# Kernel optimization log

Measured on AMD Instinct MI355X. Metric: run time of the kernel, lower is better.

The kernel has to match this reference:

```python
import jax, jax.numpy as jnp
import numpy as np

B, S, N = 64, 256, 512


def setup_inputs() -> dict:
    key = jax.random.key(0)
    ks = jax.random.split(key, 8)
    x = jax.random.normal(ks[0], (B, S, N), dtype=jnp.float32)
    # sparse adjacency, no self loops (module assumes adj has no self-loop)
    adj = (jax.random.uniform(ks[1], (N, N)) < 0.05).astype(jnp.float32)
    adj = adj * (1.0 - jnp.eye(N, dtype=jnp.float32))
    W = jax.random.uniform(ks[2], (N, N), dtype=jnp.float32)  # torch.rand init
    parent_node_weigh = jax.random.uniform(ks[3], (N,), dtype=jnp.float32)
    bound = 1.0 / np.sqrt(N)  # torch Linear default init
    Wq_w = jax.random.uniform(ks[4], (N, N), minval=-bound, maxval=bound, dtype=jnp.float32)
    Wq_b = jax.random.uniform(ks[5], (N,), minval=-bound, maxval=bound, dtype=jnp.float32)
    Wk_w = jax.random.uniform(ks[6], (N, N), minval=-bound, maxval=bound, dtype=jnp.float32)
    Wk_b = jax.random.uniform(ks[7], (N,), minval=-bound, maxval=bound, dtype=jnp.float32)
    return {"x": x, "adj": adj, "W": W, "parent_node_weigh": parent_node_weigh,
            "Wq_w": Wq_w, "Wq_b": Wq_b, "Wk_w": Wk_w, "Wk_b": Wk_b}


def reference(x, adj, W, parent_node_weigh, Wq_w, Wq_b, Wk_w, Wk_b):
    # x: (B,S,N). Q,K = Linear(x).permute(0,2,1) -> (B,N,S)
    Q = jnp.einsum('bsk,nk->bns', x, Wq_w) + Wq_b[None, :, None]
    K = jnp.einsum('bsk,nk->bns', x, Wk_w) + Wk_b[None, :, None]
    xt = jnp.transpose(x, (0, 2, 1))  # (B,N,S)
    n = adj.shape[0]
    # Algebraic equivalent of the repeat/mask/matmul/bmm chain:
    # Att[b,m,n] = adj[m,n] * sum_j W[m,j] * adj[j,n] * <K[b,j,:], Q[b,n,:]>
    S_kq = jnp.einsum('bjs,bns->bjn', K, Q)  # (B,N,N)
    Att = adj * jnp.einsum('mj,bjn->bmn', W, adj[:, :, None].transpose(2, 0, 1)[0][None] * S_kq if False else adj[None, :, :] * S_kq)
    Att = Att + jnp.diag(parent_node_weigh)[None, :, :]
    cycle_adj = jnp.eye(n, dtype=adj.dtype) + adj
    Att = jax.nn.softmax(Att, axis=1) * cycle_adj  # softmax over dim=1 (torch dim=1)
    agg_x = jnp.einsum('bmn,bms->bns', Att, xt)  # Att^T @ x
    return (agg_x, Att)
```

## Files before the change

### kernel.cpp

```cpp
#include <hip/hip_runtime.h>
#include <hip/hip_fp16.h>
#include <cstdint>
#include <cmath>

#define BB 64
#define SS 256
#define NN 512
#define MAXC 64

typedef float f32x4 __attribute__((ext_vector_type(4)));
typedef _Float16 half8 __attribute__((ext_vector_type(8)));

__device__ __forceinline__ unsigned short f2h(float f) {
  return __half_as_ushort(__float2half(f));
}
__device__ __forceinline__ float h2f(unsigned short u) {
  return __half2float(__ushort_as_half(u));
}
__device__ __forceinline__ float2 unpackh2(uint32_t u) {
  return make_float2(__half2float(__ushort_as_half((unsigned short)(u & 0xffffu))),
                     __half2float(__ushort_as_half((unsigned short)(u >> 16))));
}

__device__ __forceinline__ void gload_lds16(const void* g, void* s) {
  __builtin_amdgcn_global_load_lds(
      (const __attribute__((address_space(1))) uint32_t*)g,
      (__attribute__((address_space(3))) uint32_t*)s, 16, 0, 0);
}

__global__ __launch_bounds__(256) void k_collist(const float* __restrict__ adj,
                                                 int* __restrict__ col_idx,
                                                 int* __restrict__ col_cnt) {
  const int n = blockIdx.x * 4 + (threadIdx.x >> 6);
  const int lane = threadIdx.x & 63;
  int cnt = 0;
  for (int m0 = 0; m0 < NN; m0 += 64) {
    const int m = m0 + lane;
    const float a = adj[(size_t)m * NN + n];
    unsigned long long mask = __ballot(a != 0.0f);
    const int prefix = __popcll(mask & ((1ull << lane) - 1ull));
    if (a != 0.0f && cnt + prefix < MAXC) col_idx[n * MAXC + cnt + prefix] = m;
    cnt += __popcll(mask);
  }
  if (lane == 0) col_cnt[n] = (cnt > MAXC) ? MAXC : cnt;
}

__global__ __launch_bounds__(256) void k_wsub(const float* __restrict__ W,
                                              const int* __restrict__ col_idx,
                                              const int* __restrict__ col_cnt,
                                              int* __restrict__ col_off,
                                              float* __restrict__ Wsub) {
  const int n = blockIdx.x;
  const int t = threadIdx.x;
  const int wave = t >> 6, lane = t & 63;
  __shared__ int lsh[MAXC];
  __shared__ int preSh;
  const int c = col_cnt[n];
  if (wave == 0) {
    int pre = 0;
#pragma unroll
    for (int i0 = 0; i0 < NN; i0 += 64) {
      const int i = i0 + lane;
      const int cc = col_cnt[i];
      pre += (i < n) ? cc * cc : 0;
    }
#pragma unroll
    for (int off = 32; off; off >>= 1) pre += __shfl_xor(pre, off);
    if (lane == 0) { col_off[n] = pre; preSh = pre; }
    if (lane < c) lsh[lane] = col_idx[n * MAXC + lane];
  }
  __syncthreads();
  if (lane < c) {
    const float* Wm = W + (size_t)lsh[lane] * NN;
    float* dst = Wsub + preSh + lane;
    for (int ji = wave; ji < c; ji += 4)
      dst[(size_t)ji * c] = Wm[lsh[ji]];
  }
}

__global__ __launch_bounds__(256) void k_xprep(const float* __restrict__ x,
                                               unsigned short* __restrict__ xp,
                                               unsigned short* __restrict__ xt,
                                               float* __restrict__ Att) {
  __shared__ float tile[32][33];
  const int b = blockIdx.z;
  const int s0 = blockIdx.x * 32, n0 = blockIdx.y * 32;
  const float* xb = x + (size_t)b * SS * NN;
  const int tx = threadIdx.x, ty = threadIdx.y;
#pragma unroll
  for (int i = ty; i < 32; i += 8) {
    const float v = xb[(size_t)(s0 + i) * NN + n0 + tx];
    tile[i][tx] = v;
    xp[(size_t)(b * SS + s0 + i) * 512 + n0 + tx] = f2h(v);
  }
  {
    const int bid = (blockIdx.z * 16 + blockIdx.y) * 8 + blockIdx.x;
    const int t = ty * 32 + tx;
    f32x4* dst = (f32x4*)(Att + (size_t)bid * 2048);
    const f32x4 z = (f32x4)0.0f;
    dst[t] = z;
    dst[t + 256] = z;
  }
  __syncthreads();
  unsigned short* xtb = xt + (size_t)b * NN * SS;
#pragma unroll
  for (int i = ty; i < 32; i += 8)
    xtb[(size_t)(n0 + i) * SS + s0 + tx] = f2h(tile[tx][i]);
}

__global__ __launch_bounds__(128) void k_wsplit(const float* __restrict__ Wq,
                                                const float* __restrict__ Wk,
                                                unsigned short* __restrict__ Wqp,
                                                unsigned short* __restrict__ Wkp) {
  const int n = blockIdx.x;
  const float* src = blockIdx.y ? Wk : Wq;
  unsigned short* dst = blockIdx.y ? Wkp : Wqp;
  const int k = threadIdx.x * 4;
  float4 v = *(const float4*)(src + (size_t)n * NN + k);
  ushort4 o;
  o.x = f2h(v.x); o.y = f2h(v.y); o.z = f2h(v.z); o.w = f2h(v.w);
  *(ushort4*)(dst + (size_t)n * 512 + k) = o;
}

__global__ __launch_bounds__(256, 2) void k_lin2(const unsigned short* __restrict__ Wqp,
                                                 const unsigned short* __restrict__ Wkp,
                                                 const float* __restrict__ bq,
                                                 const float* __restrict__ bk,
                                                 const unsigned short* __restrict__ xp,
                                                 unsigned short* __restrict__ Qt,
                                                 unsigned short* __restrict__ Kt) {
  __shared__ __align__(16) char sm[49152];
  const int t = threadIdx.x;
  const int w = t >> 6, l = t & 63;
  const int id = blockIdx.x;
  const int xcd = id & 7, sub = id >> 3;
  const int bn0 = (xcd * 16 + (sub >> 2)) * 128;
  const int bm0 = (sub & 3) * 128;

  const int swz = (((l & 3) ^ ((l >> 3) & 3))) * 16;
  const char* srcb[6];
  char* dstb[6];
#pragma unroll
  for (int i = 0; i < 6; i++) {
    const int ch = w * 6 + i;
    const int panel = ch >> 3, rowgrp = ch & 7;
    const int row = rowgrp * 16 + (l >> 2);
    const char* g0 = (panel == 0) ? (const char*)Wqp
                   : (panel == 1) ? (const char*)Wkp : (const char*)xp;
    const int gr = ((panel == 2) ? bn0 : bm0) + row;
    srcb[i] = g0 + (size_t)gr * 1024 + swz;
    dstb[i] = sm + panel * 8192 + rowgrp * 1024 + l * 16;
  }

  const int fr = l & 15, fg = l >> 4;
  const int mrow = (w >> 1) * 64, ncol = (w & 1) * 64;
  const int slot = (fg ^ ((fr >> 1) & 3)) * 16;
  int offQ[4], offK[4], offB[4];
#pragma unroll
  for (int fm = 0; fm < 4; fm++) {
    offQ[fm] = (mrow + fm * 16 + fr) * 64 + slot;
    offK[fm] = 8192 + (mrow + fm * 16 + fr) * 64 + slot;
    offB[fm] = 16384 + (ncol + fm * 16 + fr) * 64 + slot;
  }

  f32x4 accq[4][4], acck[4][4];
#pragma unroll
  for (int i = 0; i < 4; i++)
#pragma unroll
    for (int j = 0; j < 4; j++) { accq[i][j] = (f32x4)0.0f; acck[i][j] = (f32x4)0.0f; }

#pragma unroll
  for (int i = 0; i < 6; i++) gload_lds16(srcb[i], dstb[i]);
  __syncthreads();

  int cur = 0;
  for (int kk = 0; kk < 16; kk++) {
    if (kk + 1 < 16) {
      const int ko = (kk + 1) * 64;
      const int boff = (cur ^ 1) * 24576;
#pragma unroll
      for (int i = 0; i < 6; i++)
        gload_lds16(srcb[i] + ko, dstb[i] + boff);
    }
    const char* base = sm + cur * 24576;
    half8 afq[4], afk[4];
#pragma unroll
    for (int fm = 0; fm < 4; fm++) {
      afq[fm] = *(const half8*)(base + offQ[fm]);
      afk[fm] = *(const half8*)(base + offK[fm]);
    }
#pragma unroll
    for (int fn = 0; fn < 4; fn++) {
      const half8 bv = *(const half8*)(base + offB[fn]);
#pragma unroll
      for (int fm = 0; fm < 4; fm++) {
        accq[fm][fn] = __builtin_amdgcn_mfma_f32_16x16x32_f16(afq[fm], bv, accq[fm][fn], 0, 0, 0);
        acck[fm][fn] = __builtin_amdgcn_mfma_f32_16x16x32_f16(afk[fm], bv, acck[fm][fn], 0, 0, 0);
      }
    }
    __syncthreads();
    cur ^= 1;
  }

  const int b = bn0 >> 8;
  const int sbase = (bn0 & 255) + ncol;
#pragma unroll
  for (int fm = 0; fm < 4; fm++) {
#pragma unroll
    for (int q = 0; q < 4; q++) {
      const int n = bm0 + mrow + fm * 16 + fg * 4 + q;
      const float bvq = bq[n];
      const float bvk = bk[n];
#pragma unroll
      for (int fn = 0; fn < 4; fn++) {
        const int s = sbase + fn * 16 + fr;
        Qt[((size_t)b * NN + n) * SS + s] = f2h(accq[fm][fn][q] + bvq);
        Kt[((size_t)b * NN + n) * SS + s] = f2h(acck[fm][fn][q] + bvk);
      }
    }
  }
}

__global__ __launch_bounds__(256, 2) void k_gram(const unsigned short* __restrict__ Qt,
                                                 const unsigned short* __restrict__ Kt,
                                                 unsigned short* __restrict__ ST) {
  __shared__ __align__(16) char sm[32768];
  const int t = threadIdx.x;
  const int w = t >> 6, l = t & 63;
  const int id = blockIdx.x;
  const int xcd = id & 7, rest = id >> 3;
  const int batch = (xcd << 3) + (rest >> 4);
  const int tile = rest & 15;
  const int m0 = (tile >> 2) * 128;
  const int n0 = (tile & 3) * 128;

  const int swz = (((l & 3) ^ ((l >> 3) & 3))) * 16;
  const char* srcb[4];
  char* dstb[4];
#pragma unroll
  for (int i = 0; i < 4; i++) {
    const int ch = w * 4 + i;
    const int panel = ch >> 3, rowgrp = ch & 7;
    const int row = rowgrp * 16 + (l >> 2);
    const char* g0 = panel ? (const char*)Kt : (const char*)Qt;
    const int gr = (panel ? n0 : m0) + row;
    srcb[i] = g0 + ((size_t)batch * 512 + gr) * 512 + swz;
    dstb[i] = sm + panel * 8192 + rowgrp * 1024 + l * 16;
  }

  const int fr = l & 15, fg = l >> 4;
  const int mrow = (w >> 1) * 64, ncol = (w & 1) * 64;
  const int slot = (fg ^ ((fr >> 1) & 3)) * 16;
  int offA[4], offB[4];
#pragma unroll
  for (int fm = 0; fm < 4; fm++) {
    offA[fm] = (mrow + fm * 16 + fr) * 64 + slot;
    offB[fm] = 8192 + (ncol + fm * 16 + fr) * 64 + slot;
  }

  f32x4 acc[4][4];
#pragma unroll
  for (int i = 0; i < 4; i++)
#pragma unroll
    for (int j = 0; j < 4; j++) acc[i][j] = (f32x4)0.0f;

#pragma unroll
  for (int i = 0; i < 4; i++) gload_lds16(srcb[i], dstb[i]);
  __syncthreads();

  int cur = 0;
  for (int kk = 0; kk < 8; kk++) {
    if (kk + 1 < 8) {
      const int ko = (kk + 1) * 64;
      const int boff = (cur ^ 1) * 16384;
#pragma unroll
      for (int i = 0; i < 4; i++)
        gload_lds16(srcb[i] + ko, dstb[i] + boff);
    }
    const char* base = sm + cur * 16384;
    half8 af[4];
#pragma unroll
    for (int fm = 0; fm < 4; fm++)
      af[fm] = *(const half8*)(base + offA[fm]);
#pragma unroll
    for (int fn = 0; fn < 4; fn++) {
      const half8 bv = *(const half8*)(base + offB[fn]);
#pragma unroll
      for (int fm = 0; fm < 4; fm++)
        acc[fm][fn] = __builtin_amdgcn_mfma_f32_16x16x32_f16(af[fm], bv, acc[fm][fn], 0, 0, 0);
    }
    __syncthreads();
    cur ^= 1;
  }

  unsigned short* STb = ST + (size_t)batch * NN * NN;
#pragma unroll
  for (int fm = 0; fm < 4; fm++) {
#pragma unroll
    for (int q = 0; q < 4; q++) {
      const int n = m0 + mrow + fm * 16 + fg * 4 + q;
#pragma unroll
      for (int fn = 0; fn < 4; fn++) {
        const int j = n0 + ncol + fn * 16 + fr;
        STb[(size_t)n * NN + j] = f2h(acc[fm][fn][q]);
      }
    }
  }
}

__global__ __launch_bounds__(256) void k_fused(const unsigned short* __restrict__ ST,
                                               const unsigned short* __restrict__ xt,
                                               const float* __restrict__ Wsub,
                                               const float* __restrict__ pnw,
                                               const int* __restrict__ col_idx,
                                               const int* __restrict__ col_cnt,
                                               const int* __restrict__ col_off,
                                               float* __restrict__ Att,
                                               float* __restrict__ agg) {
  const int id = blockIdx.x;
  const int xcd = id & 7;
  const int r = id >> 3;
  const int n = r & 511;
  const int bgrp = r >> 9;
  const int t = threadIdx.x;
  const int wave = t >> 6, lane = t & 63;
  const int b = (xcd << 3) + (bgrp << 2) + wave;

  __shared__ int   lsh[MAXC + 1];
  __shared__ int   lshB[MAXC + 1];
  __shared__ float Wsh[MAXC * MAXC];
  __shared__ float vsh[4][MAXC];
  __shared__ float ash[4][MAXC + 1];

  const int c = col_cnt[n];
  if (t < c) {
    const int v = col_idx[n * MAXC + t];
    lsh[t] = v;
    lshB[t] = v << 9;
  }
  if (t == c) { lsh[c] = n; lshB[c] = n << 9; }
  {
    const int cc = c * c;
    const float* Wp = Wsub + col_off[n];
    for (int i = t; i < cc; i += 256) Wsh[i] = Wp[i];
  }
  __syncthreads();

  const unsigned short* STrow = ST + ((size_t)b * NN + n) * NN;
  if (lane < c) vsh[wave][lane] = h2f(STrow[lsh[lane]]);

  float aval = 0.0f;
  if (lane < c) {
    for (int ji = 0; ji < c; ji++)
      aval += Wsh[ji * c + lane] * vsh[wave][ji];
  }

  const float dlg = pnw[n];
  float mval = (lane < c) ? aval : -INFINITY;
#pragma unroll
  for (int off = 32; off; off >>= 1) mval = fmaxf(mval, __shfl_xor(mval, off));
  const float colmax = fmaxf(mval, fmaxf(dlg, 0.0f));
  const float e = (lane < c) ? __expf(aval - colmax) : 0.0f;
  float sum = e;
#pragma unroll
  for (int off = 32; off; off >>= 1) sum += __shfl_xor(sum, off);
  const float denom = sum + __expf(dlg - colmax)
                    + (float)(NN - c - 1) * __expf(-colmax);
  const float inv = 1.0f / denom;

  float* Acol = Att + (size_t)b * NN * NN + n;
  if (lane < c) {
    const float attv = e * inv;
    ash[wave][lane] = attv;
    Acol[(size_t)lsh[lane] * NN] = attv;
  }
  if (lane == c) {
    const float dv = __expf(dlg - colmax) * inv;
    ash[wave][c] = dv;
    Acol[(size_t)n * NN] = dv;
  }

  const char* xtb = (const char*)(xt + (size_t)b * NN * SS);
  f32x4 acc = (f32x4)0.0f;
  for (int mi = 0; mi <= c; mi++) {
    const float a = ash[wave][mi];
    const uint2 v = *(const uint2*)(xtb + lshB[mi] + lane * 8);
    const float2 x01 = unpackh2(v.x);
    const float2 x23 = unpackh2(v.y);
    acc.x += a * x01.x;
    acc.y += a * x01.y;
    acc.z += a * x23.x;
    acc.w += a * x23.y;
  }
  *(f32x4*)(agg + ((size_t)b * NN + n) * SS + lane * 4) = acc;
}

extern "C" void kernel_launch(void* const* d_in, const int* in_sizes, int n_in,
                              void* d_out, int out_size, void* d_ws, size_t ws_size,
                              hipStream_t stream) {
  const float* x    = (const float*)d_in[0];
  const float* adj  = (const float*)d_in[1];
  const float* W    = (const float*)d_in[2];
  const float* pnw  = (const float*)d_in[3];
  const float* Wq_w = (const float*)d_in[4];
  const float* Wq_b = (const float*)d_in[5];
  const float* Wk_w = (const float*)d_in[6];
  const float* Wk_b = (const float*)d_in[7];

  float* agg = (float*)d_out;
  float* Att = (float*)d_out + (size_t)BB * NN * SS;

  char* p = (char*)d_ws;
  unsigned short* xp  = (unsigned short*)p; p += (size_t)BB * SS * 512 * 2;
  unsigned short* Wqp = (unsigned short*)p; p += (size_t)NN * 512 * 2;
  unsigned short* Wkp = (unsigned short*)p; p += (size_t)NN * 512 * 2;
  unsigned short* Qt  = (unsigned short*)p; p += (size_t)BB * NN * SS * 2;
  unsigned short* Kt  = (unsigned short*)p; p += (size_t)BB * NN * SS * 2;
  unsigned short* xt  = (unsigned short*)p; p += (size_t)BB * NN * SS * 2;
  unsigned short* ST  = (unsigned short*)p; p += (size_t)BB * NN * NN * 2;
  float* Wsub = (float*)p; p += (size_t)NN * MAXC * MAXC * 4;
  int* col_idx = (int*)p; p += (size_t)NN * MAXC * 4;
  int* col_cnt = (int*)p; p += NN * 4;
  int* col_off = (int*)p;

  k_collist<<<dim3(NN / 4), dim3(256), 0, stream>>>(adj, col_idx, col_cnt);
  k_wsub<<<dim3(NN), dim3(256), 0, stream>>>(W, col_idx, col_cnt, col_off, Wsub);
  k_xprep<<<dim3(SS / 32, NN / 32, BB), dim3(32, 8), 0, stream>>>(x, xp, xt, Att);
  k_wsplit<<<dim3(NN, 2), dim3(128), 0, stream>>>(Wq_w, Wk_w, Wqp, Wkp);

  k_lin2<<<dim3(512), dim3(256), 0, stream>>>(Wqp, Wkp, Wq_b, Wk_b, xp, Qt, Kt);
  k_gram<<<dim3(1024), dim3(256), 0, stream>>>(Qt, Kt, ST);
  k_fused<<<dim3(8192), dim3(256), 0, stream>>>(ST, xt, Wsub, pnw,
                                                col_idx, col_cnt, col_off,
                                                Att, agg);
}
```

Before: 117.0 us.

## Write sparse attention compactly then scatter rows densely in a separate pass

Instead of zero-filling the dense Att output in the prep kernel and then scattering column-strided writes from the fused kernel, the fused kernel now writes each column's nonzero attention values to a compact buffer. A new row-prep kernel builds per-row gather indices, and a new k_attw kernel assembles each dense Att row in LDS and writes it out with coalesced vector stores. This removes the strided scattered stores and the separate zero-fill. The cost is two extra launches, an extra compact buffer round trip, and a dense colpos table whose unwritten entries are never read.

Result: slower. 132.3 us (+13.1%).

```diff
diff --git a/kernel.cpp b/kernel.cpp
--- a/kernel.cpp
+++ b/kernel.cpp
@@ -7,6 +7,7 @@
 #define SS 256
 #define NN 512
 #define MAXC 64
+#define MAXC1 (MAXC + 1)
 
 typedef float f32x4 __attribute__((ext_vector_type(4)));
 typedef _Float16 half8 __attribute__((ext_vector_type(8)));
@@ -30,7 +31,8 @@
 
 __global__ __launch_bounds__(256) void k_collist(const float* __restrict__ adj,
                                                  int* __restrict__ col_idx,
-                                                 int* __restrict__ col_cnt) {
+                                                 int* __restrict__ col_cnt,
+                                                 int* __restrict__ colpos) {
   const int n = blockIdx.x * 4 + (threadIdx.x >> 6);
   const int lane = threadIdx.x & 63;
   int cnt = 0;
@@ -39,10 +41,49 @@
     const float a = adj[(size_t)m * NN + n];
     unsigned long long mask = __ballot(a != 0.0f);
     const int prefix = __popcll(mask & ((1ull << lane) - 1ull));
-    if (a != 0.0f && cnt + prefix < MAXC) col_idx[n * MAXC + cnt + prefix] = m;
+    if (a != 0.0f && cnt + prefix < MAXC) {
+      col_idx[n * MAXC + cnt + prefix] = m;
+      colpos[(size_t)m * NN + n] = cnt + prefix;
+    }
     cnt += __popcll(mask);
   }
-  if (lane == 0) col_cnt[n] = (cnt > MAXC) ? MAXC : cnt;
+  if (cnt > MAXC) cnt = MAXC;
+  if (lane == 0) {
+    col_cnt[n] = cnt;
+    colpos[(size_t)n * NN + n] = cnt;
+  }
+}
+
+__global__ __launch_bounds__(256) void k_rowprep(const float* __restrict__ adj,
+                                                 const int* __restrict__ colpos,
+                                                 int* __restrict__ rsrc_a,
+                                                 int* __restrict__ rn_a,
+                                                 int* __restrict__ nnz_row) {
+  const int m = blockIdx.x * 4 + (threadIdx.x >> 6);
+  const int wave = threadIdx.x >> 6;
+  const int lane = threadIdx.x & 63;
+  __shared__ int lsw[4][MAXC];
+  int cnt = 0;
+  for (int n0 = 0; n0 < NN; n0 += 64) {
+    const float a = adj[(size_t)m * NN + n0 + lane];
+    unsigned long long mask = __ballot(a != 0.0f);
+    const int prefix = __popcll(mask & ((1ull << lane) - 1ull));
+    if (a != 0.0f && cnt + prefix < MAXC - 1) lsw[wave][cnt + prefix] = n0 + lane;
+    cnt += __popcll(mask);
+  }
+  if (cnt > MAXC - 1) cnt = MAXC - 1;
+  if (lane < cnt) {
+    const int n = lsw[wave][lane];
+    const int pos = colpos[(size_t)m * NN + n];
+    rsrc_a[m * MAXC + lane] = n * MAXC1 + pos;
+    rn_a[m * MAXC + lane] = n;
+  }
+  if (lane == cnt) {
+    const int pos = colpos[(size_t)m * NN + m];
+    rsrc_a[m * MAXC + cnt] = m * MAXC1 + pos;
+    rn_a[m * MAXC + cnt] = m;
+    nnz_row[m] = cnt + 1;
+  }
 }
 
 __global__ __launch_bounds__(256) void k_wsub(const float* __restrict__ W,
@@ -80,8 +121,7 @@
 
 __global__ __launch_bounds__(256) void k_xprep(const float* __restrict__ x,
                                                unsigned short* __restrict__ xp,
-                                               unsigned short* __restrict__ xt,
-                                               float* __restrict__ Att) {
+                                               unsigned short* __restrict__ xt) {
   __shared__ float tile[32][33];
   const int b = blockIdx.z;
   const int s0 = blockIdx.x * 32, n0 = blockIdx.y * 32;
@@ -92,14 +132,6 @@
     const float v = xb[(size_t)(s0 + i) * NN + n0 + tx];
     tile[i][tx] = v;
     xp[(size_t)(b * SS + s0 + i) * 512 + n0 + tx] = f2h(v);
-  }
-  {
-    const int bid = (blockIdx.z * 16 + blockIdx.y) * 8 + blockIdx.x;
-    const int t = ty * 32 + tx;
-    f32x4* dst = (f32x4*)(Att + (size_t)bid * 2048);
-    const f32x4 z = (f32x4)0.0f;
-    dst[t] = z;
-    dst[t + 256] = z;
   }
   __syncthreads();
   unsigned short* xtb = xt + (size_t)b * NN * SS;
@@ -315,7 +347,7 @@
                                                const int* __restrict__ col_idx,
                                                const int* __restrict__ col_cnt,
                                                const int* __restrict__ col_off,
-                                               float* __restrict__ Att,
+                                               float* __restrict__ attv,
                                                float* __restrict__ agg) {
   const int id = blockIdx.x;
   const int xcd = id & 7;
@@ -368,16 +400,16 @@
                     + (float)(NN - c - 1) * __expf(-colmax);
   const float inv = 1.0f / denom;
 
-  float* Acol = Att + (size_t)b * NN * NN + n;
+  float* av = attv + ((size_t)b * NN + n) * MAXC1;
   if (lane < c) {
-    const float attv = e * inv;
-    ash[wave][lane] = attv;
-    Acol[(size_t)lsh[lane] * NN] = attv;
+    const float attval = e * inv;
+    ash[wave][lane] = attval;
+    av[lane] = attval;
   }
   if (lane == c) {
     const float dv = __expf(dlg - colmax) * inv;
     ash[wave][c] = dv;
-    Acol[(size_t)n * NN] = dv;
+    av[c] = dv;
   }
 
   const char* xtb = (const char*)(xt + (size_t)b * NN * SS);
@@ -395,6 +427,35 @@
   *(f32x4*)(agg + ((size_t)b * NN + n) * SS + lane * 4) = acc;
 }
 
+__global__ __launch_bounds__(256) void k_attw(const float* __restrict__ attv,
+                                              const int* __restrict__ rsrc_a,
+                                              const int* __restrict__ rn_a,
+                                              const int* __restrict__ nnz_row,
+                                              float* __restrict__ Att) {
+  const int id = blockIdx.x;
+  const int xcd = id & 7;
+  const int rest = id >> 3;
+  const int b = (xcd << 3) + (rest >> 7);
+  const int wave = threadIdx.x >> 6;
+  const int lane = threadIdx.x & 63;
+  const int m = (rest & 127) * 4 + wave;
+  __shared__ float row[4][512];
+  const f32x4 z = (f32x4)0.0f;
+  *(f32x4*)&row[wave][lane * 8] = z;
+  *(f32x4*)&row[wave][lane * 8 + 4] = z;
+  __syncthreads();
+  const int nnz = nnz_row[m];
+  if (lane < nnz) {
+    const int rs = rsrc_a[m * MAXC + lane];
+    const int rn = rn_a[m * MAXC + lane];
+    row[wave][rn] = attv[(size_t)b * (NN * MAXC1) + rs];
+  }
+  __syncthreads();
+  float* dst = Att + ((size_t)b * NN + m) * NN;
+  *(f32x4*)(dst + lane * 8)     = *(const f32x4*)&row[wave][lane * 8];
+  *(f32x4*)(dst + lane * 8 + 4) = *(const f32x4*)&row[wave][lane * 8 + 4];
+}
+
 extern "C" void kernel_launch(void* const* d_in, const int* in_sizes, int n_in,
                               void* d_out, int out_size, void* d_ws, size_t ws_size,
                               hipStream_t stream) {
@@ -419,18 +480,25 @@
   unsigned short* xt  = (unsigned short*)p; p += (size_t)BB * NN * SS * 2;
   unsigned short* ST  = (unsigned short*)p; p += (size_t)BB * NN * NN * 2;
   float* Wsub = (float*)p; p += (size_t)NN * MAXC * MAXC * 4;
+  float* attv = (float*)p; p += (size_t)BB * NN * MAXC1 * 4;
+  int* colpos = (int*)p; p += (size_t)NN * NN * 4;
   int* col_idx = (int*)p; p += (size_t)NN * MAXC * 4;
+  int* rsrc_a = (int*)p; p += (size_t)NN * MAXC * 4;
+  int* rn_a   = (int*)p; p += (size_t)NN * MAXC * 4;
   int* col_cnt = (int*)p; p += NN * 4;
+  int* nnz_row = (int*)p; p += NN * 4;
   int* col_off = (int*)p;
 
-  k_collist<<<dim3(NN / 4), dim3(256), 0, stream>>>(adj, col_idx, col_cnt);
+  k_collist<<<dim3(NN / 4), dim3(256), 0, stream>>>(adj, col_idx, col_cnt, colpos);
+  k_rowprep<<<dim3(NN / 4), dim3(256), 0, stream>>>(adj, colpos, rsrc_a, rn_a, nnz_row);
   k_wsub<<<dim3(NN), dim3(256), 0, stream>>>(W, col_idx, col_cnt, col_off, Wsub);
-  k_xprep<<<dim3(SS / 32, NN / 32, BB), dim3(32, 8), 0, stream>>>(x, xp, xt, Att);
+  k_xprep<<<dim3(SS / 32, NN / 32, BB), dim3(32, 8), 0, stream>>>(x, xp, xt);
   k_wsplit<<<dim3(NN, 2), dim3(128), 0, stream>>>(Wq_w, Wk_w, Wqp, Wkp);
 
   k_lin2<<<dim3(512), dim3(256), 0, stream>>>(Wqp, Wkp, Wq_b, Wk_b, xp, Qt, Kt);
   k_gram<<<dim3(1024), dim3(256), 0, stream>>>(Qt, Kt, ST);
   k_fused<<<dim3(8192), dim3(256), 0, stream>>>(ST, xt, Wsub, pnw,
                                                 col_idx, col_cnt, col_off,
-                                                Att, agg);
-}
+                                                attv, agg);
+  k_attw<<<dim3(8192), dim3(256), 0, stream>>>(attv, rsrc_a, rn_a, nnz_row, Att);
+}
```
